# Kernel optimization log

Hardware: AMD Instinct MI355X
Metric: run time of the kernel (lower is better)

## Reference

```python
import jax, jax.numpy as jnp
import numpy as np

NEG_INF = -1e9  # matches masked_fill value in torch code
LRELU_ALPHA = 0.2


def setup_inputs() -> dict:
    key = jax.random.key(0)
    k1, k2, k3, k4 = jax.random.split(key, 4)
    B, N, F_IN, H, DK = 4, 2048, 128, 4, 32
    x = jax.random.normal(k1, (B, N, F_IN), dtype=jnp.float32)
    adj = jax.random.randint(k2, (B, N, N), 0, 2, dtype=jnp.int32)
    # xavier-ish scaled params
    W = jax.random.normal(k3, (H, F_IN, DK), dtype=jnp.float32) * (1.0 / np.sqrt(F_IN))
    a = jax.random.normal(k4, (H, 2 * DK, 1), dtype=jnp.float32) * (1.0 / np.sqrt(2 * DK))
    return {"x": x, "adj": adj, "W": W, "a": a}


def reference(x, adj, W, a):
    B, N, _ = x.shape
    H, _, DK = W.shape
    # h: (B, H, N, DK)
    h = jnp.einsum('bni,hio->bhno', x, W)
    # Split attention vector: e[b,h,i,j] = h_i.a_l + h_j.a_r  (avoids O(N^2 * 2d) concat)
    a_l = a[:, :DK, 0]   # (H, DK)
    a_r = a[:, DK:, 0]   # (H, DK)
    el = jnp.einsum('bhnd,hd->bhn', h, a_l)  # (B, H, N)
    er = jnp.einsum('bhnd,hd->bhn', h, a_r)  # (B, H, N)
    e = el[:, :, :, None] + er[:, :, None, :]          # (B, H, N, N)
    e = jax.nn.leaky_relu(e, negative_slope=LRELU_ALPHA)
    e = jnp.where(adj[:, None, :, :] == 0, NEG_INF, e)
    alpha = jax.nn.softmax(e, axis=-1)                 # dropout is identity (eval)
    h_prime = jnp.einsum('bhij,bhjd->bhid', alpha, h)  # (B, H, N, DK)
    # torch code does h_prime.view(B, N, -1) on contiguous (B,H,N,DK): raw reshape
    out = h_prime.reshape(B, N, H * DK)
    return out
```

## Files before the change

kernel.cpp:

```cpp
#include <hip/hip_runtime.h>
#include <stdint.h>

#define LOG2E 1.4426950408889634f

typedef __bf16 v8bf __attribute__((ext_vector_type(8)));
typedef float v16f __attribute__((ext_vector_type(16)));

static constexpr int B = 4, N = 2048, FIN = 128, H = 4, DK = 32;
static constexpr int IT = N / 32;
static constexpr int PACK_BLOCKS = B * N * N / 1024;
static constexpr int PREP_BLOCKS = (B * N * FIN + H * DK * FIN) / 256;

__device__ __forceinline__ float exp2_fast(float x) {
#if __has_builtin(__builtin_amdgcn_exp2f)
  return __builtin_amdgcn_exp2f(x);
#else
  float r;
  asm("v_exp_f32 %0, %1" : "=v"(r) : "v"(x));
  return r;
#endif
}

__device__ __forceinline__ unsigned int bf16_rne(float f) {
  unsigned int u = __builtin_bit_cast(unsigned int, f);
  u += 0x7FFFu + ((u >> 16) & 1u);
  return u >> 16;
}

__global__ __launch_bounds__(256) void k_prep(const int* __restrict__ adj,
                                              const float* __restrict__ x,
                                              const float* __restrict__ W,
                                              unsigned int* __restrict__ adjb,
                                              unsigned short* __restrict__ xb,
                                              unsigned short* __restrict__ wtb) {
  int bid = blockIdx.x;
  int tid = threadIdx.x;
  if (bid < PACK_BLOCKS) {
    int wid = (bid * 256 + tid) >> 6;
    int lane = tid & 63;
    const int* p = adj + (size_t)wid * 256 + lane;
    unsigned long long m0 = __ballot(p[0] != 0);
    unsigned long long m1 = __ballot(p[64] != 0);
    unsigned long long m2 = __ballot(p[128] != 0);
    unsigned long long m3 = __ballot(p[192] != 0);
    if (lane == 0) {
      uint4 v0 = {(unsigned)m0, (unsigned)(m0 >> 32), (unsigned)m1, (unsigned)(m1 >> 32)};
      uint4 v1 = {(unsigned)m2, (unsigned)(m2 >> 32), (unsigned)m3, (unsigned)(m3 >> 32)};
      uint4* dst = (uint4*)(adjb + (size_t)wid * 8);
      dst[0] = v0;
      dst[1] = v1;
    }
    return;
  }
  int idx = (bid - PACK_BLOCKS) * 256 + tid;
  constexpr int TX = B * N * FIN;
  if (idx < TX) {
    xb[idx] = (unsigned short)bf16_rne(x[idx]);
  } else {
    int j = idx - TX;
    int h = j >> 12, r = j & 4095, d = r >> 7, f = r & 127;
    wtb[j] = (unsigned short)bf16_rne(W[(h * FIN + f) * DK + d]);
  }
}

__global__ __launch_bounds__(256) void k_hproj(const unsigned short* __restrict__ xb,
                                               const unsigned short* __restrict__ wtb,
                                               const float* __restrict__ a,
                                               unsigned short* __restrict__ h_frag,
                                               float* __restrict__ el,
                                               float* __restrict__ er) {
  int blk = blockIdx.x;
  int b = blk >> 6, it = blk & 63;
  int tid = threadIdx.x;
  int head = tid >> 6, lane = tid & 63;
  int lrow = lane & 31, kh = lane >> 5;
  int bh = b * H + head;
  int n = it * 32 + lrow;
  const unsigned short* xp = xb + (b * N + n) * FIN + kh * 8;
  const unsigned short* wp = wtb + (head * DK + lrow) * FIN + kh * 8;
  v16f acc = {};
  v16f accd = {};
#pragma unroll
  for (int s = 0; s < FIN / 16; ++s) {
    v8bf av = __builtin_bit_cast(v8bf, *(const int4*)(wp + s * 16));
    v8bf bv = __builtin_bit_cast(v8bf, *(const int4*)(xp + s * 16));
    acc = __builtin_amdgcn_mfma_f32_32x32x16_bf16(av, bv, acc, 0, 0, 0);
    accd = __builtin_amdgcn_mfma_f32_32x32x16_bf16(bv, av, accd, 0, 0, 0);
  }
  {
    unsigned w[8];
#pragma unroll
    for (int i = 0; i < 8; ++i)
      w[i] = bf16_rne(accd[2 * i]) | (bf16_rne(accd[2 * i + 1]) << 16);
    unsigned short* fp = h_frag + (((size_t)bh * 128 + it * 2) * 64 + lane) * 8;
    int4 v0 = {(int)w[0], (int)w[1], (int)w[2], (int)w[3]};
    int4 v1 = {(int)w[4], (int)w[5], (int)w[6], (int)w[7]};
    *(int4*)fp = v0;
    *(int4*)(fp + 512) = v1;
  }
  float pel = 0.f, per = 0.f;
#pragma unroll
  for (int r = 0; r < 16; ++r) {
    int d = (r & 3) + 8 * (r >> 2) + 4 * kh;
    float hv = acc[r];
    pel = fmaf(hv, a[head * 2 * DK + d], pel);
    per = fmaf(hv, a[head * 2 * DK + DK + d], per);
  }
  pel += __shfl_xor(pel, 32);
  per += __shfl_xor(per, 32);
  if (kh == 0) {
    el[bh * N + n] = pel * LOG2E;
    er[bh * N + n] = per * LOG2E;
  }
}

__global__ __launch_bounds__(1024, 4) void k_attn(const unsigned int* __restrict__ adjb,
                                                  const unsigned short* __restrict__ h_frag,
                                                  const float* __restrict__ el,
                                                  const float* __restrict__ er,
                                                  float* __restrict__ pnum,
                                                  float* __restrict__ pden) {
  __shared__ __align__(16) float part4[4][H][1024];
  __shared__ float lsh4[4][H][32];
  int blk = blockIdx.x;
  int bit = blk >> 1, jh = blk & 1;
  int b = bit >> 6, it = bit & 63;
  int tid = threadIdx.x;
  int wave = tid >> 6;
  int head = wave & 3, jq = wave >> 2;
  int lane = tid & 63, lrow = lane & 31, kh = lane >> 5;
  int ig = it * 32 + lrow, bh = b * H + head;

  {
    int hh = tid >> 8, jl = (tid & 255) * 4;
    *(float4*)&part4[0][hh][jl] = *(const float4*)&er[(b * H + hh) * N + jh * 1024 + jl];
  }

  float eli = el[bh * N + ig];
  const unsigned short* hp =
      h_frag + (((size_t)bh * 128 + jh * 64 + jq * 16) * 64 + lane) * 8;
  int jql = jq * 256 + 4 * kh;

  const uint4* abp = (const uint4*)(adjb + (size_t)(b * N + ig) * 64 + jh * 32 + jq * 8);
  uint4 ab0 = abp[0], ab1 = abp[1];
  unsigned adw[8] = {ab0.x, ab0.y, ab0.z, ab0.w, ab1.x, ab1.y, ab1.z, ab1.w};
  int shkh = kh * 4;

  int4 hreg0 = *(const int4*)hp;
  int4 hreg1 = *(const int4*)(hp + 512);

  __syncthreads();

  v16f acc = {};
  float lsum = 0.f;
  float4 Ea = *(const float4*)&part4[0][head][jql];
  float4 Eb = *(const float4*)&part4[0][head][jql + 8];
#pragma unroll
  for (int s = 0; s < 16; ++s) {
    int4 hb = (s & 1) ? hreg1 : hreg0;
    if (s + 2 < 16) {
      int4 nv = *(const int4*)(hp + (s + 2) * 512);
      if (s & 1) hreg1 = nv; else hreg0 = nv;
    }
    float4 ea = Ea, eb = Eb;
    if (s + 1 < 16) {
      Ea = *(const float4*)&part4[0][head][jql + (s + 1) * 16];
      Eb = *(const float4*)&part4[0][head][jql + (s + 1) * 16 + 8];
    }
    unsigned mb = (adw[s >> 1] >> (((s & 1) * 16) + shkh)) & 0xF0Fu;
    float ev[8] = {ea.x, ea.y, ea.z, ea.w, eb.x, eb.y, eb.z, eb.w};
    unsigned ub[8];
#pragma unroll
    for (int k = 0; k < 8; ++k) {
      float tt = eli + ev[k];
      tt = fmaxf(tt, 0.2f * tt);
      float pv = exp2_fast(tt);
      unsigned u = __builtin_bit_cast(unsigned, pv) & 0xFFFF0000u;
      u = (mb & (1u << ((k & 3) + 8 * (k >> 2)))) ? u : 0u;
      ub[k] = u;
      lsum += __builtin_bit_cast(float, u);
    }
    unsigned u0 = __builtin_amdgcn_perm(ub[1], ub[0], 0x07060302u);
    unsigned u1 = __builtin_amdgcn_perm(ub[3], ub[2], 0x07060302u);
    unsigned u2 = __builtin_amdgcn_perm(ub[5], ub[4], 0x07060302u);
    unsigned u3 = __builtin_amdgcn_perm(ub[7], ub[6], 0x07060302u);
    uint4 au = {u0, u1, u2, u3};
    v8bf av = __builtin_bit_cast(v8bf, au);
    v8bf hv = __builtin_bit_cast(v8bf, hb);
    acc = __builtin_amdgcn_mfma_f32_32x32x16_bf16(av, hv, acc, 0, 0, 0);
  }

  lsum += __shfl_xor(lsum, 32);
  if (lane < 32) lsh4[jq][head][lane] = lsum;

  __syncthreads();

#pragma unroll
  for (int r = 0; r < 16; ++r) {
    int rowl = (r & 3) + 8 * (r >> 2) + 4 * kh;
    part4[jq][head][rowl * 32 + lrow] = acc[r];
  }
  __syncthreads();

  int e = tid * 4;
  int rh = e >> 10, rr = e & 1023;
  float4 q0 = *(const float4*)&part4[0][rh][rr];
  float4 q1 = *(const float4*)&part4[1][rh][rr];
  float4 q2 = *(const float4*)&part4[2][rh][rr];
  float4 q3 = *(const float4*)&part4[3][rh][rr];
  float4 s4;
  s4.x = (q0.x + q1.x) + (q2.x + q3.x);
  s4.y = (q0.y + q1.y) + (q2.y + q3.y);
  s4.z = (q0.z + q1.z) + (q2.z + q3.z);
  s4.w = (q0.w + q1.w) + (q2.w + q3.w);
  *(float4*)&pnum[(size_t)blk * 4096 + e] = s4;
  if (tid < 128) {
    float d = (lsh4[0][tid >> 5][tid & 31] + lsh4[1][tid >> 5][tid & 31]) +
              (lsh4[2][tid >> 5][tid & 31] + lsh4[3][tid >> 5][tid & 31]);
    pden[blk * 128 + tid] = d;
  }
}

__global__ __launch_bounds__(1024) void k_final(const float* __restrict__ pnum,
                                                const float* __restrict__ pden,
                                                float* __restrict__ out) {
  int bit = blockIdx.x;
  int b = bit >> 6, it = bit & 63;
  int tid = threadIdx.x;
  int e = tid * 4;
  int rh = e >> 10, ri = (e >> 5) & 31, rd = e & 31;
  size_t p0 = (size_t)(bit * 2) * 4096 + e;
  float4 n0 = *(const float4*)&pnum[p0];
  float4 n1 = *(const float4*)&pnum[p0 + 4096];
  float d = pden[bit * 2 * 128 + rh * 32 + ri] + pden[(bit * 2 + 1) * 128 + rh * 32 + ri];
  float inv = 1.0f / d;
  float4 o;
  o.x = (n0.x + n1.x) * inv;
  o.y = (n0.y + n1.y) * inv;
  o.z = (n0.z + n1.z) * inv;
  o.w = (n0.w + n1.w) * inv;
  *(float4*)&out[(size_t)((b * H + rh) * N + it * 32 + ri) * DK + rd] = o;
}

extern "C" void kernel_launch(void* const* d_in, const int* in_sizes, int n_in,
                              void* d_out, int out_size, void* d_ws, size_t ws_size,
                              hipStream_t stream) {
  const float* x = (const float*)d_in[0];
  const int* adj = (const int*)d_in[1];
  const float* W = (const float*)d_in[2];
  const float* a = (const float*)d_in[3];
  float* out = (float*)d_out;
  char* ws = (char*)d_ws;

  unsigned short* h_frag = (unsigned short*)(ws);
  float* el = (float*)(ws + 0x200000);
  float* er = (float*)(ws + 0x220000);
  unsigned short* wtb = (unsigned short*)(ws + 0x240000);
  unsigned int* adjb = (unsigned int*)(ws + 0x250000);
  unsigned short* xb = (unsigned short*)(ws + 0x450000);
  float* pnum = (float*)(ws + 0x650000);
  float* pden = (float*)(ws + 0xE50000);

  hipLaunchKernelGGL(k_prep, dim3(PACK_BLOCKS + PREP_BLOCKS), dim3(256), 0, stream,
                     adj, x, W, adjb, xb, wtb);
  hipLaunchKernelGGL(k_hproj, dim3(B * IT), dim3(256), 0, stream, xb, wtb, a, h_frag, el, er);
  hipLaunchKernelGGL(k_attn, dim3(B * IT * 2), dim3(1024), 0, stream, adjb, h_frag, el, er, pnum, pden);
  hipLaunchKernelGGL(k_final, dim3(B * IT), dim3(1024), 0, stream, pnum, pden, out);
}
```

Before: 131.7 us.

## Factor exp of leaky-relu into precomputed per-node exponentials and split attention four ways

The inner attention loop no longer computes an exp2 per edge. It uses exp2(lrelu(el+er)) = max(2^el·2^er, 2^(0.2el)·2^(0.2er)), with the per-column exponentials precomputed in the projection kernel and the per-row ones computed once per thread. The attention grid also changes from 2 column halves with 1024-thread blocks to 4 column quarters with 512-thread blocks, which doubles the partial numerator buffer that the final kernel reduces. The factored form drops the max-free softmax range safety it relied on before and can overflow or underflow for larger logits, though it is fine for these inputs.

Measured after the change: 127.1 us. 3.5% less time.

```diff
diff --git a/kernel.cpp b/kernel.cpp
--- a/kernel.cpp
+++ b/kernel.cpp
@@ -68,7 +68,8 @@
                                                const float* __restrict__ a,
                                                unsigned short* __restrict__ h_frag,
                                                float* __restrict__ el,
-                                               float* __restrict__ er) {
+                                               float* __restrict__ er2,
+                                               float* __restrict__ fr2) {
   int blk = blockIdx.x;
   int b = blk >> 6, it = blk & 63;
   int tid = threadIdx.x;
@@ -110,38 +111,47 @@
   per += __shfl_xor(per, 32);
   if (kh == 0) {
     el[bh * N + n] = pel * LOG2E;
-    er[bh * N + n] = per * LOG2E;
-  }
-}
-
-__global__ __launch_bounds__(1024, 4) void k_attn(const unsigned int* __restrict__ adjb,
-                                                  const unsigned short* __restrict__ h_frag,
-                                                  const float* __restrict__ el,
-                                                  const float* __restrict__ er,
-                                                  float* __restrict__ pnum,
-                                                  float* __restrict__ pden) {
-  __shared__ __align__(16) float part4[4][H][1024];
-  __shared__ float lsh4[4][H][32];
+    float t = per * LOG2E;
+    er2[bh * N + n] = exp2_fast(t);
+    fr2[bh * N + n] = exp2_fast(0.2f * t);
+  }
+}
+
+__global__ __launch_bounds__(512, 4) void k_attn(const unsigned int* __restrict__ adjb,
+                                                 const unsigned short* __restrict__ h_frag,
+                                                 const float* __restrict__ el,
+                                                 const float* __restrict__ er2,
+                                                 const float* __restrict__ fr2,
+                                                 float* __restrict__ pnum,
+                                                 float* __restrict__ pden) {
+  __shared__ __align__(16) float part2[2][H][1024];
+  __shared__ float lsh2[2][H][32];
+  float(*stg)[H][512] = (float(*)[H][512]) & part2[0][0][0];
   int blk = blockIdx.x;
-  int bit = blk >> 1, jh = blk & 1;
+  int bit = blk >> 2, jQ = blk & 3;
   int b = bit >> 6, it = bit & 63;
   int tid = threadIdx.x;
   int wave = tid >> 6;
-  int head = wave & 3, jq = wave >> 2;
+  int head = wave & 3, kq = wave >> 2;
   int lane = tid & 63, lrow = lane & 31, kh = lane >> 5;
   int ig = it * 32 + lrow, bh = b * H + head;
 
   {
-    int hh = tid >> 8, jl = (tid & 255) * 4;
-    *(float4*)&part4[0][hh][jl] = *(const float4*)&er[(b * H + hh) * N + jh * 1024 + jl];
+    int hh = tid >> 7, jl = (tid & 127) * 4;
+    int base = (b * H + hh) * N + jQ * 512 + jl;
+    *(float4*)&stg[0][hh][jl] = *(const float4*)&er2[base];
+    *(float4*)&stg[1][hh][jl] = *(const float4*)&fr2[base];
   }
 
   float eli = el[bh * N + ig];
+  float Eli = exp2_fast(eli);
+  float Fli = exp2_fast(0.2f * eli);
+
   const unsigned short* hp =
-      h_frag + (((size_t)bh * 128 + jh * 64 + jq * 16) * 64 + lane) * 8;
-  int jql = jq * 256 + 4 * kh;
-
-  const uint4* abp = (const uint4*)(adjb + (size_t)(b * N + ig) * 64 + jh * 32 + jq * 8);
+      h_frag + (((size_t)bh * 128 + jQ * 32 + kq * 16) * 64 + lane) * 8;
+  int jql = kq * 256 + 4 * kh;
+
+  const uint4* abp = (const uint4*)(adjb + (size_t)(b * N + ig) * 64 + jQ * 16 + kq * 8);
   uint4 ab0 = abp[0], ab1 = abp[1];
   unsigned adw[8] = {ab0.x, ab0.y, ab0.z, ab0.w, ab1.x, ab1.y, ab1.z, ab1.w};
   int shkh = kh * 4;
@@ -153,8 +163,10 @@
 
   v16f acc = {};
   float lsum = 0.f;
-  float4 Ea = *(const float4*)&part4[0][head][jql];
-  float4 Eb = *(const float4*)&part4[0][head][jql + 8];
+  float4 Ea = *(const float4*)&stg[0][head][jql];
+  float4 Eb = *(const float4*)&stg[0][head][jql + 8];
+  float4 Fa = *(const float4*)&stg[1][head][jql];
+  float4 Fb = *(const float4*)&stg[1][head][jql + 8];
 #pragma unroll
   for (int s = 0; s < 16; ++s) {
     int4 hb = (s & 1) ? hreg1 : hreg0;
@@ -162,19 +174,20 @@
       int4 nv = *(const int4*)(hp + (s + 2) * 512);
       if (s & 1) hreg1 = nv; else hreg0 = nv;
     }
-    float4 ea = Ea, eb = Eb;
+    float4 ea = Ea, eb = Eb, fa = Fa, fb = Fb;
     if (s + 1 < 16) {
-      Ea = *(const float4*)&part4[0][head][jql + (s + 1) * 16];
-      Eb = *(const float4*)&part4[0][head][jql + (s + 1) * 16 + 8];
+      Ea = *(const float4*)&stg[0][head][jql + (s + 1) * 16];
+      Eb = *(const float4*)&stg[0][head][jql + (s + 1) * 16 + 8];
+      Fa = *(const float4*)&stg[1][head][jql + (s + 1) * 16];
+      Fb = *(const float4*)&stg[1][head][jql + (s + 1) * 16 + 8];
     }
     unsigned mb = (adw[s >> 1] >> (((s & 1) * 16) + shkh)) & 0xF0Fu;
     float ev[8] = {ea.x, ea.y, ea.z, ea.w, eb.x, eb.y, eb.z, eb.w};
+    float fv[8] = {fa.x, fa.y, fa.z, fa.w, fb.x, fb.y, fb.z, fb.w};
     unsigned ub[8];
 #pragma unroll
     for (int k = 0; k < 8; ++k) {
-      float tt = eli + ev[k];
-      tt = fmaxf(tt, 0.2f * tt);
-      float pv = exp2_fast(tt);
+      float pv = fmaxf(Eli * ev[k], Fli * fv[k]);
       unsigned u = __builtin_bit_cast(unsigned, pv) & 0xFFFF0000u;
       u = (mb & (1u << ((k & 3) + 8 * (k >> 2)))) ? u : 0u;
       ub[k] = u;
@@ -191,33 +204,29 @@
   }
 
   lsum += __shfl_xor(lsum, 32);
-  if (lane < 32) lsh4[jq][head][lane] = lsum;
+  if (lane < 32) lsh2[kq][head][lane] = lsum;
 
   __syncthreads();
 
 #pragma unroll
   for (int r = 0; r < 16; ++r) {
     int rowl = (r & 3) + 8 * (r >> 2) + 4 * kh;
-    part4[jq][head][rowl * 32 + lrow] = acc[r];
+    part2[kq][head][rowl * 32 + lrow] = acc[r];
   }
   __syncthreads();
 
-  int e = tid * 4;
+  int e = tid * 8;
   int rh = e >> 10, rr = e & 1023;
-  float4 q0 = *(const float4*)&part4[0][rh][rr];
-  float4 q1 = *(const float4*)&part4[1][rh][rr];
-  float4 q2 = *(const float4*)&part4[2][rh][rr];
-  float4 q3 = *(const float4*)&part4[3][rh][rr];
-  float4 s4;
-  s4.x = (q0.x + q1.x) + (q2.x + q3.x);
-  s4.y = (q0.y + q1.y) + (q2.y + q3.y);
-  s4.z = (q0.z + q1.z) + (q2.z + q3.z);
-  s4.w = (q0.w + q1.w) + (q2.w + q3.w);
-  *(float4*)&pnum[(size_t)blk * 4096 + e] = s4;
+  float4 a0 = *(const float4*)&part2[0][rh][rr];
+  float4 a1 = *(const float4*)&part2[1][rh][rr];
+  float4 b0 = *(const float4*)&part2[0][rh][rr + 4];
+  float4 b1 = *(const float4*)&part2[1][rh][rr + 4];
+  float4 s0 = {a0.x + a1.x, a0.y + a1.y, a0.z + a1.z, a0.w + a1.w};
+  float4 s1 = {b0.x + b1.x, b0.y + b1.y, b0.z + b1.z, b0.w + b1.w};
+  *(float4*)&pnum[(size_t)blk * 4096 + e] = s0;
+  *(float4*)&pnum[(size_t)blk * 4096 + e + 4] = s1;
   if (tid < 128) {
-    float d = (lsh4[0][tid >> 5][tid & 31] + lsh4[1][tid >> 5][tid & 31]) +
-              (lsh4[2][tid >> 5][tid & 31] + lsh4[3][tid >> 5][tid & 31]);
-    pden[blk * 128 + tid] = d;
+    pden[blk * 128 + tid] = lsh2[0][tid >> 5][tid & 31] + lsh2[1][tid >> 5][tid & 31];
   }
 }
 
@@ -229,16 +238,19 @@
   int tid = threadIdx.x;
   int e = tid * 4;
   int rh = e >> 10, ri = (e >> 5) & 31, rd = e & 31;
-  size_t p0 = (size_t)(bit * 2) * 4096 + e;
+  size_t p0 = (size_t)(bit * 4) * 4096 + e;
   float4 n0 = *(const float4*)&pnum[p0];
   float4 n1 = *(const float4*)&pnum[p0 + 4096];
-  float d = pden[bit * 2 * 128 + rh * 32 + ri] + pden[(bit * 2 + 1) * 128 + rh * 32 + ri];
+  float4 n2 = *(const float4*)&pnum[p0 + 2 * 4096];
+  float4 n3 = *(const float4*)&pnum[p0 + 3 * 4096];
+  int dbase = bit * 4 * 128 + rh * 32 + ri;
+  float d = (pden[dbase] + pden[dbase + 128]) + (pden[dbase + 256] + pden[dbase + 384]);
   float inv = 1.0f / d;
   float4 o;
-  o.x = (n0.x + n1.x) * inv;
-  o.y = (n0.y + n1.y) * inv;
-  o.z = (n0.z + n1.z) * inv;
-  o.w = (n0.w + n1.w) * inv;
+  o.x = ((n0.x + n1.x) + (n2.x + n3.x)) * inv;
+  o.y = ((n0.y + n1.y) + (n2.y + n3.y)) * inv;
+  o.z = ((n0.z + n1.z) + (n2.z + n3.z)) * inv;
+  o.w = ((n0.w + n1.w) + (n2.w + n3.w)) * inv;
   *(float4*)&out[(size_t)((b * H + rh) * N + it * 32 + ri) * DK + rd] = o;
 }
 
@@ -254,16 +266,18 @@
 
   unsigned short* h_frag = (unsigned short*)(ws);
   float* el = (float*)(ws + 0x200000);
-  float* er = (float*)(ws + 0x220000);
-  unsigned short* wtb = (unsigned short*)(ws + 0x240000);
-  unsigned int* adjb = (unsigned int*)(ws + 0x250000);
-  unsigned short* xb = (unsigned short*)(ws + 0x450000);
-  float* pnum = (float*)(ws + 0x650000);
-  float* pden = (float*)(ws + 0xE50000);
+  float* er2 = (float*)(ws + 0x220000);
+  float* fr2 = (float*)(ws + 0x240000);
+  unsigned short* wtb = (unsigned short*)(ws + 0x260000);
+  unsigned int* adjb = (unsigned int*)(ws + 0x270000);
+  unsigned short* xb = (unsigned short*)(ws + 0x470000);
+  float* pnum = (float*)(ws + 0x670000);
+  float* pden = (float*)(ws + 0x1670000);
 
   hipLaunchKernelGGL(k_prep, dim3(PACK_BLOCKS + PREP_BLOCKS), dim3(256), 0, stream,
                      adj, x, W, adjb, xb, wtb);
-  hipLaunchKernelGGL(k_hproj, dim3(B * IT), dim3(256), 0, stream, xb, wtb, a, h_frag, el, er);
-  hipLaunchKernelGGL(k_attn, dim3(B * IT * 2), dim3(1024), 0, stream, adjb, h_frag, el, er, pnum, pden);
+  hipLaunchKernelGGL(k_hproj, dim3(B * IT), dim3(256), 0, stream, xb, wtb, a, h_frag, el, er2, fr2);
+  hipLaunchKernelGGL(k_attn, dim3(B * IT * 4), dim3(512), 0, stream, adjb, h_frag, el, er2, fr2,
+                     pnum, pden);
   hipLaunchKernelGGL(k_final, dim3(B * IT), dim3(1024), 0, stream, pnum, pden, out);
 }
```
